# Kernel tuning notes

Hardware: AMD Instinct MI355X
Metric: run time of the kernel (lower is better)

## Reference

```python
import jax, jax.numpy as jnp
import numpy as np

IN_F = 512
OUT_F = 768
B = OUT_F - IN_F  # 256 discrimination features
I = 16            # intermediate features
N = 256           # batch size


def setup_inputs() -> dict:
    key = jax.random.key(0)
    kx, kT = jax.random.split(key)
    x = jax.random.normal(kx, (N, IN_F), dtype=jnp.float32)
    T = jax.random.normal(kT, (IN_F, B, I), dtype=jnp.float32) * 0.02
    return {"x": x, "T": T}


def reference(x, T):
    # M: (N, B, I) = x @ T reshaped
    M = jnp.einsum('nf,fbi->nbi', x, T)
    # pairwise L1 distance over intermediate dim: (N, N, B)
    l1 = jnp.abs(M[:, None, :, :] - M[None, :, :, :]).sum(axis=3)
    # exp-sum over the pair dim; torch sums over dim=0 of (M - M_t) where
    # M has leading unsqueeze(0) -> equivalent to summing over j here.
    out = jnp.exp(-l1).sum(axis=0) - 1.0  # (N, B); subtract self-pair
    return jnp.concatenate([x, out], axis=1)  # (N, OUT_F)
```

## Files before the change

### kernel.cpp

```cpp
#include <hip/hip_runtime.h>
#include <stdint.h>

#define IN_F 512
#define OUT_F 768
#define BD 256
#define ID 16
#define ND 256
#define CD 4096
#define MS 20

typedef __bf16 bf16x8 __attribute__((ext_vector_type(8)));
typedef float f32x4 __attribute__((ext_vector_type(4)));

__device__ __forceinline__ unsigned short f2bf(float f) {
    union { float f; uint32_t u; } v; v.f = f;
    uint32_t u = v.u + 0x7FFFu + ((v.u >> 16) & 1u);
    return (unsigned short)(u >> 16);
}

__device__ __forceinline__ unsigned sad16(unsigned a, unsigned b, unsigned c) {
    unsigned d;
    asm("v_sad_u16 %0, %1, %2, %3" : "=v"(d) : "v"(a), "v"(b), "v"(c));
    return d;
}

__global__ __launch_bounds__(256) void xprep_kernel(const float* __restrict__ x,
                                                    unsigned short* __restrict__ xbf,
                                                    float* __restrict__ out) {
    const int bid = blockIdx.x;
    const int t = threadIdx.x;
    if (bid < 128) {
        int i0 = (bid * 256 + t) * 8;
        float4 a = *reinterpret_cast<const float4*>(x + i0);
        float4 c = *reinterpret_cast<const float4*>(x + i0 + 4);
        union { unsigned short s[8]; uint4 v; } u;
        u.s[0] = f2bf(a.x); u.s[1] = f2bf(a.y); u.s[2] = f2bf(a.z); u.s[3] = f2bf(a.w);
        u.s[4] = f2bf(c.x); u.s[5] = f2bf(c.y); u.s[6] = f2bf(c.z); u.s[7] = f2bf(c.w);
        *reinterpret_cast<uint4*>(xbf + i0) = u.v;
    } else {
        int r = (bid - 128) * 2 + (t >> 7);
        int q = t & 127;
        float4 v = reinterpret_cast<const float4*>(x + (size_t)r * IN_F)[q];
        reinterpret_cast<float4*>(out + (size_t)r * OUT_F)[q] = v;
    }
}

__global__ __launch_bounds__(1024) void mbd_fused3(const unsigned short* __restrict__ xbf,
                                                   const float* __restrict__ T,
                                                   float* __restrict__ out) {
    __shared__ __align__(16) unsigned char smem[32768 + 16384 + 8192];
    float* Tst = (float*)smem;
    unsigned short* Tfrag = (unsigned short*)(smem + 32768);
    unsigned short* Mq = (unsigned short*)(smem + 32768 + 16384);
    float* red = (float*)smem;

    const int b = blockIdx.x;
    const int t = threadIdx.x;
    const int lane = t & 63;
    const int w = t >> 6;
    const int rc = lane & 15;
    const int g = lane >> 4;

#pragma unroll
    for (int s = 0; s < 2; ++s) {
        int q = s * 1024 + t;
        int f = q >> 2, c4 = (q & 3) << 2;
        float4 v = *reinterpret_cast<const float4*>(T + (size_t)f * CD + b * ID + c4);
        *reinterpret_cast<float4*>(&Tst[f * ID + c4]) = v;
    }
    __syncthreads();

    {
        const int kg = t >> 4;
        const int c = t & 15;
        union { unsigned short s[8]; uint4 v; } p;
#pragma unroll
        for (int e = 0; e < 8; ++e) p.s[e] = f2bf(Tst[(kg * 8 + e) * ID + c]);
        *reinterpret_cast<uint4*>(Tfrag + (size_t)t * 8) = p.v;
    }
    __syncthreads();

    const bf16x8* Av = reinterpret_cast<const bf16x8*>(xbf);
    const bf16x8* Bf = reinterpret_cast<const bf16x8*>(Tfrag);
    const int arow = w * 16 + rc;
    f32x4 acc = {0.f, 0.f, 0.f, 0.f};
#pragma unroll 4
    for (int k = 0; k < 16; ++k) {
        bf16x8 afr = Av[(size_t)arow * 64 + k * 4 + g];
        bf16x8 bfr = Bf[(k * 4 + g) * 16 + rc];
        acc = __builtin_amdgcn_mfma_f32_16x16x32_bf16(afr, bfr, acc, 0, 0, 0);
    }
#pragma unroll
    for (int r = 0; r < 4; ++r) {
        float q = (acc[r] + 8.0f) * 4096.0f + 0.5f;
        q = fminf(fmaxf(q, 0.0f), 65535.0f);
        Mq[(w * 16 + g * 4 + r) * ID + rc] = (unsigned short)(unsigned int)q;
    }
    __syncthreads();

    const uint4* Mq4 = reinterpret_cast<const uint4*>(Mq);
    uint4 ma[4][2];
#pragma unroll
    for (int r = 0; r < 4; ++r) {
        const int row = lane + 64 * r;
        ma[r][0] = Mq4[row * 2];
        ma[r][1] = Mq4[row * 2 + 1];
    }

    const float K = -1.44269504f / 4096.0f;
    float pacc[4] = {0.f, 0.f, 0.f, 0.f};
    const int j0 = w * 16;
#pragma unroll 2
    for (int j = j0; j < j0 + 16; ++j) {
        uint4 blo = Mq4[j * 2];
        uint4 bhi = Mq4[j * 2 + 1];
#pragma unroll
        for (int r = 0; r < 4; ++r) {
            unsigned s = 0;
            s = sad16(ma[r][0].x, blo.x, s);
            s = sad16(ma[r][0].y, blo.y, s);
            s = sad16(ma[r][0].z, blo.z, s);
            s = sad16(ma[r][0].w, blo.w, s);
            s = sad16(ma[r][1].x, bhi.x, s);
            s = sad16(ma[r][1].y, bhi.y, s);
            s = sad16(ma[r][1].z, bhi.z, s);
            s = sad16(ma[r][1].w, bhi.w, s);
            pacc[r] += exp2f((float)s * K);
        }
    }
#pragma unroll
    for (int r = 0; r < 4; ++r) red[w * ND + lane + 64 * r] = pacc[r];
    __syncthreads();

    if (t < ND) {
        float s = -1.0f;
#pragma unroll
        for (int w2 = 0; w2 < 16; ++w2) s += red[w2 * ND + t];
        out[(size_t)t * OUT_F + IN_F + b] = s;
    }
}

__global__ __launch_bounds__(256) void mbd_one(const float* __restrict__ x,
                                               const float* __restrict__ T,
                                               float* __restrict__ out) {
    __shared__ float Tsh[IN_F * ID];
    __shared__ float Msh[ND * MS];
    const int b = blockIdx.x;
    const int t = threadIdx.x;
    const int lane = t & 63;
    const int w = t >> 6;
#pragma unroll
    for (int s = 0; s < 8; ++s) {
        int q = s * 256 + t;
        int f = q >> 2, c4 = (q & 3) << 2;
        float4 v = *reinterpret_cast<const float4*>(T + (size_t)f * CD + b * ID + c4);
        *reinterpret_cast<float4*>(&Tsh[f * ID + c4]) = v;
    }
    __syncthreads();
    const int rc = lane & 15;
    const int g = lane >> 4;
    f32x4 acc[4];
#pragma unroll
    for (int i = 0; i < 4; ++i) acc[i] = f32x4{0.f, 0.f, 0.f, 0.f};
    const float* xw = x + (size_t)(w * 64 + rc) * IN_F;
    for (int k = 0; k < 16; ++k) {
        bf16x8 bfr;
#pragma unroll
        for (int e = 0; e < 8; ++e) bfr[e] = (__bf16)Tsh[(k * 32 + g * 8 + e) * ID + rc];
        const int xo = k * 32 + g * 8;
#pragma unroll
        for (int nt = 0; nt < 4; ++nt) {
            const float* ap = xw + (size_t)nt * 16 * IN_F + xo;
            float4 a0 = *reinterpret_cast<const float4*>(ap);
            float4 a1 = *reinterpret_cast<const float4*>(ap + 4);
            bf16x8 afr;
            afr[0] = (__bf16)a0.x; afr[1] = (__bf16)a0.y;
            afr[2] = (__bf16)a0.z; afr[3] = (__bf16)a0.w;
            afr[4] = (__bf16)a1.x; afr[5] = (__bf16)a1.y;
            afr[6] = (__bf16)a1.z; afr[7] = (__bf16)a1.w;
            acc[nt] = __builtin_amdgcn_mfma_f32_16x16x32_bf16(afr, bfr, acc[nt], 0, 0, 0);
        }
    }
#pragma unroll
    for (int nt = 0; nt < 4; ++nt)
#pragma unroll
        for (int r = 0; r < 4; ++r)
            Msh[((w * 4 + nt) * 16 + g * 4 + r) * MS + rc] = acc[nt][r];
    __syncthreads();
    float mr[4][ID];
#pragma unroll
    for (int r = 0; r < 4; ++r)
#pragma unroll
        for (int ii = 0; ii < 4; ++ii) {
            float4 v = *reinterpret_cast<const float4*>(&Msh[(lane + 64 * r) * MS + ii * 4]);
            mr[r][ii * 4] = v.x; mr[r][ii * 4 + 1] = v.y;
            mr[r][ii * 4 + 2] = v.z; mr[r][ii * 4 + 3] = v.w;
        }
    float pacc[4] = {0.f, 0.f, 0.f, 0.f};
    const int j0 = w * 64;
#pragma unroll 2
    for (int j = j0; j < j0 + 64; ++j) {
        float mj[ID];
#pragma unroll
        for (int ii = 0; ii < 4; ++ii) {
            float4 v = *reinterpret_cast<const float4*>(&Msh[j * MS + ii * 4]);
            mj[ii * 4] = v.x; mj[ii * 4 + 1] = v.y;
            mj[ii * 4 + 2] = v.z; mj[ii * 4 + 3] = v.w;
        }
#pragma unroll
        for (int r = 0; r < 4; ++r) {
            float s0 = 0.f, s1 = 0.f, s2 = 0.f, s3 = 0.f;
#pragma unroll
            for (int i = 0; i < ID; i += 4) {
                s0 += fabsf(mr[r][i + 0] - mj[i + 0]);
                s1 += fabsf(mr[r][i + 1] - mj[i + 1]);
                s2 += fabsf(mr[r][i + 2] - mj[i + 2]);
                s3 += fabsf(mr[r][i + 3] - mj[i + 3]);
            }
            pacc[r] += __expf(-((s0 + s1) + (s2 + s3)));
        }
    }
    float* red = Tsh;
#pragma unroll
    for (int r = 0; r < 4; ++r) red[w * 256 + lane + 64 * r] = pacc[r];
    __syncthreads();
    {
        float s = red[t] + red[256 + t] + red[512 + t] + red[768 + t] - 1.0f;
        out[(size_t)t * OUT_F + IN_F + b] = s;
    }
    if (t < IN_F / 4) {
        float4 v = reinterpret_cast<const float4*>(x + (size_t)b * IN_F)[t];
        reinterpret_cast<float4*>(out + (size_t)b * OUT_F)[t] = v;
    }
}

extern "C" void kernel_launch(void* const* d_in, const int* in_sizes, int n_in,
                              void* d_out, int out_size, void* d_ws, size_t ws_size,
                              hipStream_t stream) {
    const float* x = (const float*)d_in[0];
    const float* T = (const float*)d_in[1];
    float* out = (float*)d_out;

    const size_t needed = (size_t)ND * IN_F * 2;

    if (ws_size >= needed) {
        unsigned short* xbf = (unsigned short*)d_ws;
        xprep_kernel<<<dim3(256), dim3(256), 0, stream>>>(x, xbf, out);
        mbd_fused3<<<dim3(BD), dim3(1024), 0, stream>>>(xbf, T, out);
    } else {
        mbd_one<<<dim3(BD), dim3(256), 0, stream>>>(x, T, out);
    }
}
```

Baseline: 27.62 us.

## Quantize M to 8-bit, use v_sad_u8 and an LDS exp lookup table

M values are now quantized to unsigned 8-bit with an offset of 3 and a scale of 42.5, where before they were 16-bit. This packs 16 features into one uint4, so each pairwise L1 distance takes 4 v_sad_u8 instructions instead of 8. The per-pair exp2f is replaced by a lookup in a 4096-entry table of exponentials kept in LDS, and the pair loop unroll is raised. The change cuts ALU and LDS traffic in the pairwise stage. In exchange it adds coarser quantization error, clamps any M value outside ±3, and risks LDS bank conflicts on the data-dependent table reads.

```diff
diff --git a/kernel.cpp b/kernel.cpp
--- a/kernel.cpp
+++ b/kernel.cpp
@@ -9,6 +9,8 @@
 #define CD 4096
 #define MS 20
 
+#define QSCALE 42.5f
+
 typedef __bf16 bf16x8 __attribute__((ext_vector_type(8)));
 typedef float f32x4 __attribute__((ext_vector_type(4)));
 
@@ -18,9 +20,9 @@
     return (unsigned short)(u >> 16);
 }
 
-__device__ __forceinline__ unsigned sad16(unsigned a, unsigned b, unsigned c) {
+__device__ __forceinline__ unsigned sad8(unsigned a, unsigned b, unsigned c) {
     unsigned d;
-    asm("v_sad_u16 %0, %1, %2, %3" : "=v"(d) : "v"(a), "v"(b), "v"(c));
+    asm("v_sad_u8 %0, %1, %2, %3" : "=v"(d) : "v"(a), "v"(b), "v"(c));
     return d;
 }
 
@@ -45,14 +47,15 @@
     }
 }
 
-__global__ __launch_bounds__(1024) void mbd_fused3(const unsigned short* __restrict__ xbf,
+__global__ __launch_bounds__(1024) void mbd_fused4(const unsigned short* __restrict__ xbf,
                                                    const float* __restrict__ T,
                                                    float* __restrict__ out) {
-    __shared__ __align__(16) unsigned char smem[32768 + 16384 + 8192];
+    __shared__ __align__(16) unsigned char smem[32768 + 16384 + 4096];
     float* Tst = (float*)smem;
+    float* LUT = (float*)smem;
+    float* red = (float*)smem + 4096;
     unsigned short* Tfrag = (unsigned short*)(smem + 32768);
-    unsigned short* Mq = (unsigned short*)(smem + 32768 + 16384);
-    float* red = (float*)smem;
+    unsigned char* Mq = smem + 32768 + 16384;
 
     const int b = blockIdx.x;
     const int t = threadIdx.x;
@@ -79,6 +82,15 @@
         *reinterpret_cast<uint4*>(Tfrag + (size_t)t * 8) = p.v;
     }
     __syncthreads();
+
+    {
+        const float K = -1.44269504f / QSCALE;
+#pragma unroll
+        for (int u = 0; u < 4; ++u) {
+            int idx = t * 4 + u;
+            LUT[idx] = exp2f((float)idx * K);
+        }
+    }
 
     const bf16x8* Av = reinterpret_cast<const bf16x8*>(xbf);
     const bf16x8* Bf = reinterpret_cast<const bf16x8*>(Tfrag);
@@ -92,40 +104,30 @@
     }
 #pragma unroll
     for (int r = 0; r < 4; ++r) {
-        float q = (acc[r] + 8.0f) * 4096.0f + 0.5f;
-        q = fminf(fmaxf(q, 0.0f), 65535.0f);
-        Mq[(w * 16 + g * 4 + r) * ID + rc] = (unsigned short)(unsigned int)q;
+        float q = (acc[r] + 3.0f) * QSCALE + 0.5f;
+        q = fminf(fmaxf(q, 0.0f), 255.0f);
+        Mq[(w * 16 + g * 4 + r) * ID + rc] = (unsigned char)(unsigned int)q;
     }
     __syncthreads();
 
     const uint4* Mq4 = reinterpret_cast<const uint4*>(Mq);
-    uint4 ma[4][2];
-#pragma unroll
-    for (int r = 0; r < 4; ++r) {
-        const int row = lane + 64 * r;
-        ma[r][0] = Mq4[row * 2];
-        ma[r][1] = Mq4[row * 2 + 1];
-    }
-
-    const float K = -1.44269504f / 4096.0f;
+    uint4 ma[4];
+#pragma unroll
+    for (int r = 0; r < 4; ++r) ma[r] = Mq4[lane + 64 * r];
+
     float pacc[4] = {0.f, 0.f, 0.f, 0.f};
     const int j0 = w * 16;
-#pragma unroll 2
+#pragma unroll 4
     for (int j = j0; j < j0 + 16; ++j) {
-        uint4 blo = Mq4[j * 2];
-        uint4 bhi = Mq4[j * 2 + 1];
+        uint4 mb = Mq4[j];
 #pragma unroll
         for (int r = 0; r < 4; ++r) {
             unsigned s = 0;
-            s = sad16(ma[r][0].x, blo.x, s);
-            s = sad16(ma[r][0].y, blo.y, s);
-            s = sad16(ma[r][0].z, blo.z, s);
-            s = sad16(ma[r][0].w, blo.w, s);
-            s = sad16(ma[r][1].x, bhi.x, s);
-            s = sad16(ma[r][1].y, bhi.y, s);
-            s = sad16(ma[r][1].z, bhi.z, s);
-            s = sad16(ma[r][1].w, bhi.w, s);
-            pacc[r] += exp2f((float)s * K);
+            s = sad8(ma[r].x, mb.x, s);
+            s = sad8(ma[r].y, mb.y, s);
+            s = sad8(ma[r].z, mb.z, s);
+            s = sad8(ma[r].w, mb.w, s);
+            pacc[r] += LUT[s];
         }
     }
 #pragma unroll
@@ -246,7 +248,7 @@
     if (ws_size >= needed) {
         unsigned short* xbf = (unsigned short*)d_ws;
         xprep_kernel<<<dim3(256), dim3(256), 0, stream>>>(x, xbf, out);
-        mbd_fused3<<<dim3(BD), dim3(1024), 0, stream>>>(xbf, T, out);
+        mbd_fused4<<<dim3(BD), dim3(1024), 0, stream>>>(xbf, T, out);
     } else {
         mbd_one<<<dim3(BD), dim3(256), 0, stream>>>(x, T, out);
     }
```

Result: faster. 23.66 us (-14.3%).
